# Kernel optimization log

Measured on AMD Instinct MI355X. Metric: run time of the kernel, lower is better.

Reference implementation:

```python
import jax, jax.numpy as jnp
import numpy as np

D_IN = 1024
D_OUT = 1024
NUM_HEADS = 16
HEAD_DIM = D_OUT // NUM_HEADS


def setup_inputs() -> dict:
    key = jax.random.key(0)
    ks = jax.random.split(key, 6)
    s = 0.02
    return {
        "x": jax.random.normal(ks[0], (4, 2048, D_IN), dtype=jnp.float32),
        "W_q": jax.random.normal(ks[1], (D_IN, D_OUT), dtype=jnp.float32) * s,
        "W_k": jax.random.normal(ks[2], (D_IN, D_OUT), dtype=jnp.float32) * s,
        "W_v": jax.random.normal(ks[3], (D_IN, D_OUT), dtype=jnp.float32) * s,
        "W_o": jax.random.normal(ks[4], (D_OUT, D_OUT), dtype=jnp.float32) * s,
        "b_o": jax.random.normal(ks[5], (D_OUT,), dtype=jnp.float32) * s,
    }


def reference(x, W_q, W_k, W_v, W_o, b_o):
    b, n, _ = x.shape
    # project and split heads: [b, h, n, d]
    q = (x @ W_q).reshape(b, n, NUM_HEADS, HEAD_DIM).transpose(0, 2, 1, 3)
    k = (x @ W_k).reshape(b, n, NUM_HEADS, HEAD_DIM).transpose(0, 2, 1, 3)
    v = (x @ W_v).reshape(b, n, NUM_HEADS, HEAD_DIM).transpose(0, 2, 1, 3)
    scores = jnp.einsum("bhqd,bhkd->bhqk", q, k)
    causal = jnp.tril(jnp.ones((n, n), dtype=bool))  # True = keep
    scores = jnp.where(causal, scores, -jnp.inf)
    attn = jax.nn.softmax(scores / np.sqrt(HEAD_DIM).astype(np.float32), axis=-1)
    ctx = jnp.einsum("bhqk,bhkd->bhqd", attn, v)
    ctx = ctx.transpose(0, 2, 1, 3).reshape(b, n, D_OUT)
    return ctx @ W_o + b_o
```

## Files before the change

kernel.cpp:

```cpp
#include <hip/hip_runtime.h>
#include <hip/hip_bf16.h>

#define NHEADS 16
#define HDIM 64
#define SEQ 2048
#define BATCH 4
#define DMODEL 1024
#define MTOT (BATCH * SEQ)

typedef short v8s __attribute__((ext_vector_type(8)));
typedef short v4s __attribute__((ext_vector_type(4)));
typedef float v4f __attribute__((ext_vector_type(4)));
typedef float v16f __attribute__((ext_vector_type(16)));
typedef unsigned int v4u __attribute__((ext_vector_type(4)));
typedef unsigned short u16;
typedef unsigned int u32;

__device__ __forceinline__ u16 f2bf(float f) {
    union { float f; unsigned u; } v; v.f = f;
    unsigned r = v.u + 0x7FFFu + ((v.u >> 16) & 1u);
    return (u16)(r >> 16);
}

__device__ __forceinline__ void g2l16(const u16* g, short* l) {
    __builtin_amdgcn_global_load_lds(
        (const __attribute__((address_space(1))) u32*)g,
        (__attribute__((address_space(3))) u32*)l, 16, 0, 0);
}

__device__ __forceinline__ unsigned pk_bf16(float a, float b) {
    unsigned r;
    asm("v_cvt_pk_bf16_f32 %0, %1, %2" : "=v"(r) : "v"(a), "v"(b));
    return r;
}
__device__ __forceinline__ void pl32swap(unsigned& x, unsigned& y) {
    asm("v_permlane32_swap_b32 %0, %1" : "+v"(x), "+v"(y));
}
__device__ __forceinline__ v8s build_pa(float a0, float a1, float a2, float a3,
                                        float b0, float b1, float b2, float b3) {
    unsigned X  = pk_bf16(a0, a1);
    unsigned X2 = pk_bf16(a2, a3);
    unsigned Y  = pk_bf16(b0, b1);
    unsigned Y2 = pk_bf16(b2, b3);
    pl32swap(X, Y);
    pl32swap(X2, Y2);
    v4u w; w[0] = X; w[1] = X2; w[2] = Y; w[3] = Y2;
    return __builtin_bit_cast(v8s, w);
}

__device__ __forceinline__ void transpose_body(
    const float* __restrict__ src, u16* __restrict__ dst, int k0, int n0)
{
    __shared__ __align__(8) short Ts[64 * 68];
    const int t = threadIdx.x;
    const int n4 = (t & 15) * 4, kl = t >> 4;
#pragma unroll
    for (int it = 0; it < 4; ++it) {
        int k = kl + 16 * it;
        v4f v = *(const v4f*)&src[(size_t)(k0 + k) * DMODEL + n0 + n4];
        v4s p;
#pragma unroll
        for (int e = 0; e < 4; ++e) p[e] = (short)f2bf(v[e]);
        *(v4s*)&Ts[k * 68 + n4] = p;
    }
    __syncthreads();
    const int nl = t >> 4, k4 = (t & 15) * 4;
#pragma unroll
    for (int it = 0; it < 4; ++it) {
        int n = nl + 16 * it;
        v4s o;
#pragma unroll
        for (int e = 0; e < 4; ++e) o[e] = Ts[(k4 + e) * 68 + n];
        *(v4s*)&dst[(size_t)(n0 + n) * DMODEL + k0 + k4] = o;
    }
}

__global__ __launch_bounds__(256)
void transpose_w(const float* __restrict__ src, u16* __restrict__ dst)
{
    transpose_body(src, dst, blockIdx.x * 64, blockIdx.y * 64);
}

__global__ __launch_bounds__(256)
void prep(const float* __restrict__ x, u16* __restrict__ xb,
          const float* __restrict__ s0, const float* __restrict__ s1,
          const float* __restrict__ s2, const float* __restrict__ s3,
          u16* __restrict__ wdst)
{
    const int blk = blockIdx.x;
    if (blk < 1024) {
        const int z = blk >> 8;
        const int rem = blk & 255;
        const float* src = (z == 0) ? s0 : (z == 1) ? s1 : (z == 2) ? s2 : s3;
        transpose_body(src, wdst + (size_t)z * DMODEL * DMODEL,
                       (rem & 15) * 64, (rem >> 4) * 64);
    } else {
        size_t i = ((size_t)(blk - 1024) * 256 + threadIdx.x) * 8;
        v4f a = *(const v4f*)&x[i];
        v4f b = *(const v4f*)&x[i + 4];
        v8s p;
#pragma unroll
        for (int e = 0; e < 4; ++e) p[e] = (short)f2bf(a[e]);
#pragma unroll
        for (int e = 0; e < 4; ++e) p[4 + e] = (short)f2bf(b[e]);
        *(v8s*)&xb[i] = p;
    }
}

#define QSCALE (0.125f * 1.44269504088896f)

__device__ __forceinline__ void qkv_epilogue(
    v4f (&acc)[4][4], int which, int n0, int m0, int wn, int wm,
    int l15, int quad, u16* Qb, u16* Kb, u16* Vt)
{
    if (which == 2) {
#pragma unroll
        for (int i = 0; i < 4; ++i)
#pragma unroll
            for (int j = 0; j < 4; ++j) {
                int col = n0 + wn + j * 16 + l15;
                int h = col >> 6, d = col & 63;
                int m = m0 + wm + i * 16 + quad * 4;
                int b = m >> 11, n = m & (SEQ - 1);
                v4s pv;
#pragma unroll
                for (int r = 0; r < 4; ++r) pv[r] = (short)f2bf(acc[i][j][r]);
                *(v4s*)&Vt[((size_t)(b * NHEADS + h) * HDIM + d) * SEQ + n] = pv;
            }
    } else {
        u16* Ob = (which == 0) ? Qb : Kb;
        const float scale = (which == 0) ? QSCALE : 1.0f;
#pragma unroll
        for (int i = 0; i < 4; ++i)
#pragma unroll
            for (int j = 0; j < 4; ++j) {
                int col = n0 + wn + j * 16 + l15;
                int h = col >> 6, d = col & 63;
#pragma unroll
                for (int r = 0; r < 4; ++r) {
                    int m = m0 + wm + i * 16 + quad * 4 + r;
                    int b = m >> 11, n = m & (SEQ - 1);
                    Ob[((size_t)(b * NHEADS + h) * SEQ + n) * HDIM + d] =
                        f2bf(acc[i][j][r] * scale);
                }
            }
    }
}

#define QKV_ABUF (256 * 64)
#define QKV_BBUF (128 * 64)

__device__ __forceinline__ void qkv_stage(
    const u16* __restrict__ xb, const u16* __restrict__ W,
    int m0, int t, int s, short* As3, short* Bs3)
{
    const int srr = t >> 3;
    const int scol = ((t & 7) ^ (srr & 7)) * 8;
    short* A = As3 + (s % 3) * QKV_ABUF;
    short* B = Bs3 + (s % 3) * QKV_BBUF;
    const int k0 = s * 64;
#pragma unroll
    for (int c = 0; c < 4; ++c)
        g2l16(&xb[(size_t)(m0 + c * 64 + srr) * DMODEL + k0 + scol],
              &A[(c * 64 + srr) * 64 + (t & 7) * 8]);
#pragma unroll
    for (int c = 0; c < 2; ++c)
        g2l16(&W[(size_t)(c * 64 + srr) * DMODEL + k0 + scol],
              &B[(c * 64 + srr) * 64 + (t & 7) * 8]);
}

__global__ __launch_bounds__(512, 1)
void qkv_fast(const u16* __restrict__ xb, const u16* __restrict__ Wt,
              u16* __restrict__ Qb, u16* __restrict__ Kb, u16* __restrict__ Vt)
{
    __shared__ __align__(16) short As3[3 * QKV_ABUF];
    __shared__ __align__(16) short Bs3[3 * QKV_BBUF];

    const int bx = blockIdx.x;
    const int which = bx >> 3;
    const int n0 = (bx & 7) * 128;
    const int m0 = blockIdx.y * 256;
    const u16* W = Wt + (size_t)which * DMODEL * DMODEL + (size_t)n0 * DMODEL;

    const int t = threadIdx.x;
    const int lane = t & 63;
    const int l15 = lane & 15;
    const int quad = lane >> 4;
    const int wave = t >> 6;
    const int wm = (wave >> 1) * 64;
    const int wn = (wave & 1) * 64;

    v4f acc[4][4];
#pragma unroll
    for (int i = 0; i < 4; ++i)
#pragma unroll
        for (int j = 0; j < 4; ++j) acc[i][j] = {0.f, 0.f, 0.f, 0.f};

    qkv_stage(xb, W, m0, t, 0, As3, Bs3);
    qkv_stage(xb, W, m0, t, 1, As3, Bs3);

#pragma unroll 1
    for (int tt = 0; tt < 16; ++tt) {
        if (tt < 15) asm volatile("s_waitcnt vmcnt(6)" ::: "memory");
        else         asm volatile("s_waitcnt vmcnt(0)" ::: "memory");
        __builtin_amdgcn_sched_barrier(0);
        __builtin_amdgcn_s_barrier();
        __builtin_amdgcn_sched_barrier(0);

        if (tt + 2 < 16) qkv_stage(xb, W, m0, t, tt + 2, As3, Bs3);

        const short* A = As3 + (tt % 3) * QKV_ABUF;
        const short* B = Bs3 + (tt % 3) * QKV_BBUF;
        v8s af[4][2], bf[4][2];
#pragma unroll
        for (int i = 0; i < 4; ++i)
#pragma unroll
            for (int kh = 0; kh < 2; ++kh)
                af[i][kh] = *(const v8s*)&A[(wm + i * 16 + l15) * 64 +
                                            (((kh * 4 + quad) ^ (l15 & 7)) << 3)];
#pragma unroll
        for (int j = 0; j < 4; ++j)
#pragma unroll
            for (int kh = 0; kh < 2; ++kh)
                bf[j][kh] = *(const v8s*)&B[(wn + j * 16 + l15) * 64 +
                                            (((kh * 4 + quad) ^ (l15 & 7)) << 3)];
        __builtin_amdgcn_s_setprio(1);
#pragma unroll
        for (int i = 0; i < 4; ++i)
#pragma unroll
            for (int j = 0; j < 4; ++j)
#pragma unroll
                for (int kh = 0; kh < 2; ++kh)
                    acc[i][j] = __builtin_amdgcn_mfma_f32_16x16x32_bf16(
                        af[i][kh], bf[j][kh], acc[i][j], 0, 0, 0);
        __builtin_amdgcn_s_setprio(0);
    }

    qkv_epilogue(acc, which, n0, m0, wn, wm, l15, quad, Qb, Kb, Vt);
}

__global__ __launch_bounds__(256, 2)
void qkv_slow(const float* __restrict__ x, const u16* __restrict__ Wt,
              u16* __restrict__ Qb, u16* __restrict__ Kb, u16* __restrict__ Vt)
{
    __shared__ __align__(16) short As[128 * 32];
    __shared__ __align__(16) short Bs[128 * 32];

    const int which = blockIdx.z;
    const u16* W = Wt + (size_t)which * DMODEL * DMODEL;

    const int n0 = blockIdx.x * 128;
    const int m0 = blockIdx.y * 128;
    const int t = threadIdx.x;
    const int lane = t & 63;
    const int l15 = lane & 15;
    const int quad = lane >> 4;
    const int wave = t >> 6;
    const int wm = (wave >> 1) * 64;
    const int wn = (wave & 1) * 64;
    const int srow = t >> 2;
    const int sc8 = (t & 3) * 8;

    v4f acc[4][4];
#pragma unroll
    for (int i = 0; i < 4; ++i)
#pragma unroll
        for (int j = 0; j < 4; ++j) acc[i][j] = {0.f, 0.f, 0.f, 0.f};

    for (int k0 = 0; k0 < DMODEL; k0 += 32) {
        __syncthreads();
        g2l16(&W[(size_t)(n0 + srow) * DMODEL + k0 + sc8], &Bs[srow * 32 + sc8]);
        g2l16(&W[(size_t)(n0 + 64 + srow) * DMODEL + k0 + sc8],
              &Bs[(64 + srow) * 32 + sc8]);
#pragma unroll
        for (int it = 0; it < 2; ++it) {
            int row = srow + 64 * it;
            const float* xp = &x[(size_t)(m0 + row) * DMODEL + k0 + sc8];
            v4f x0 = *(const v4f*)xp;
            v4f x1 = *(const v4f*)(xp + 4);
            v8s av;
#pragma unroll
            for (int e = 0; e < 4; ++e) av[e] = (short)f2bf(x0[e]);
#pragma unroll
            for (int e = 0; e < 4; ++e) av[4 + e] = (short)f2bf(x1[e]);
            *(v8s*)&As[row * 32 + sc8] = av;
        }
        __syncthreads();

        v8s af[4], bf[4];
#pragma unroll
        for (int i = 0; i < 4; ++i)
            af[i] = *(const v8s*)&As[(wm + i * 16 + l15) * 32 + quad * 8];
#pragma unroll
        for (int j = 0; j < 4; ++j)
            bf[j] = *(const v8s*)&Bs[(wn + j * 16 + l15) * 32 + quad * 8];
#pragma unroll
        for (int i = 0; i < 4; ++i)
#pragma unroll
            for (int j = 0; j < 4; ++j)
                acc[i][j] = __builtin_amdgcn_mfma_f32_16x16x32_bf16(
                    af[i], bf[j], acc[i][j], 0, 0, 0);
    }
    qkv_epilogue(acc, which, n0, m0, wn, wm, l15, quad, Qb, Kb, Vt);
}

#define VXOR(d) ((((d) & 7) << 1) | (((d) >> 3) & 1))

__global__ __launch_bounds__(256, 2)
void attn(const u16* __restrict__ Qb, const u16* __restrict__ Kb,
          const u16* __restrict__ Vt, u16* __restrict__ Cx)
{
    __shared__ __align__(16) short Ks[128 * 64];
    __shared__ __align__(16) short Vs[64 * 128];

    const int ell = blockIdx.x;
    const int xcd = ell & 7;
    const int rest = ell >> 3;
    const int p = rest & 7;
    const int bh = ((rest >> 3) << 3) | xcd;

    const int t = threadIdx.x;
    const int lane = t & 63;
    const int l31 = lane & 31;
    const int hi = lane >> 5;
    const int wave = t >> 6;
    const int koff = hi * 8;

    const u16* Qh = Qb + (size_t)bh * SEQ * HDIM;
    const u16* Kh = Kb + (size_t)bh * SEQ * HDIM;
    const u16* Vh = Vt + (size_t)bh * HDIM * SEQ;

    const int krow = t >> 3;
    const int kslot = t & 7;
    const int vrow = t >> 4;
    const int vslot = t & 15;
    const int b = bh >> 4, h = bh & 15;

#pragma unroll 1
    for (int phase = 0; phase < 2; ++phase) {
        const int qt = phase ? p : (15 - p);
        const int q0w = qt * 128 + wave * 32;

        v8s qf[4];
#pragma unroll
        for (int dc = 0; dc < 4; ++dc)
            qf[dc] = *(const v8s*)
                &Qh[(size_t)(q0w + l31) * HDIM + dc * 16 + koff];

        v16f o0, o1;
#pragma unroll
        for (int r = 0; r < 16; ++r) { o0[r] = 0.f; o1[r] = 0.f; }
        float ls = 0.f;

        v8s pk[4], pv[4];
#pragma unroll
        for (int it = 0; it < 4; ++it)
            pk[it] = *(const v8s*)
                &Kh[(size_t)(it * 32 + krow) * HDIM + kslot * 8];
#pragma unroll
        for (int it = 0; it < 4; ++it)
            pv[it] = *(const v8s*)
                &Vh[(size_t)(it * 16 + vrow) * SEQ + vslot * 8];

#pragma unroll 1
        for (int kb = 0; kb <= qt; ++kb) {
            __syncthreads();
#pragma unroll
            for (int it = 0; it < 4; ++it) {
                int row = it * 32 + krow;
                *(v8s*)&Ks[row * 64 + ((kslot ^ (row & 7)) << 3)] = pk[it];
            }
#pragma unroll
            for (int it = 0; it < 4; ++it) {
                int d = it * 16 + vrow;
                *(v8s*)&Vs[d * 128 + ((vslot ^ VXOR(d)) << 3)] = pv[it];
            }
            __syncthreads();

            if (kb < qt) {
                const int kn = (kb + 1) * 128;
#pragma unroll
                for (int it = 0; it < 4; ++it)
                    pk[it] = *(const v8s*)
                        &Kh[(size_t)(kn + it * 32 + krow) * HDIM + kslot * 8];
#pragma unroll
                for (int it = 0; it < 4; ++it)
                    pv[it] = *(const v8s*)
                        &Vh[(size_t)(it * 16 + vrow) * SEQ + kn + vslot * 8];
            }

#pragma unroll
            for (int k2 = 0; k2 < 2; ++k2) {
                const int kbase = kb * 128 + k2 * 64;
                if (kbase > q0w + 31) continue;
                const bool diag = (kbase + 63 > q0w);
                const int qrow = q0w + l31;

                v16f st0, st1;
#pragma unroll
                for (int r = 0; r < 16; ++r) { st0[r] = 0.f; st1[r] = 0.f; }
#pragma unroll
                for (int dc = 0; dc < 4; ++dc) {
                    const int ds = dc * 2 + hi;
                    const int r0 = k2 * 64 + l31;
                    const int r1 = k2 * 64 + 32 + l31;
                    v8s kf0 = *(const v8s*)
                        &Ks[r0 * 64 + ((ds ^ (r0 & 7)) << 3)];
                    v8s kf1 = *(const v8s*)
                        &Ks[r1 * 64 + ((ds ^ (r1 & 7)) << 3)];
                    st0 = __builtin_amdgcn_mfma_f32_32x32x16_bf16(
                        kf0, qf[dc], st0, 0, 0, 0);
                    st1 = __builtin_amdgcn_mfma_f32_32x32x16_bf16(
                        kf1, qf[dc], st1, 0, 0, 0);
                }

                v16f pe0, pe1;
                if (!diag) {
#pragma unroll
                    for (int r = 0; r < 16; ++r) {
                        pe0[r] = exp2f(st0[r]);
                        pe1[r] = exp2f(st1[r]);
                    }
                } else {
#pragma unroll
                    for (int r = 0; r < 16; ++r) {
                        int kl = kbase + (r & 3) + 8 * (r >> 2) + 4 * hi;
                        pe0[r] = (kl > qrow) ? 0.f : exp2f(st0[r]);
                        pe1[r] = (kl + 32 > qrow) ? 0.f : exp2f(st1[r]);
                    }
                }
#pragma unroll
                for (int r = 0; r < 16; ++r) ls += pe0[r] + pe1[r];

                v8s pa0 = build_pa(pe0[0], pe0[1], pe0[2], pe0[3],
                                   pe0[4], pe0[5], pe0[6], pe0[7]);
                v8s pa1 = build_pa(pe0[8], pe0[9], pe0[10], pe0[11],
                                   pe0[12], pe0[13], pe0[14], pe0[15]);
                v8s pa2 = build_pa(pe1[0], pe1[1], pe1[2], pe1[3],
                                   pe1[4], pe1[5], pe1[6], pe1[7]);
                v8s pa3 = build_pa(pe1[8], pe1[9], pe1[10], pe1[11],
                                   pe1[12], pe1[13], pe1[14], pe1[15]);

#pragma unroll
                for (int kc = 0; kc < 4; ++kc) {
                    v8s pav = (kc == 0) ? pa0 : (kc == 1) ? pa1
                              : (kc == 2) ? pa2 : pa3;
                    const int ks = k2 * 8 + kc * 2 + hi;
                    const int d0 = l31, d1 = 32 + l31;
                    v8s vf0 = *(const v8s*)
                        &Vs[d0 * 128 + ((ks ^ VXOR(d0)) << 3)];
                    v8s vf1 = *(const v8s*)
                        &Vs[d1 * 128 + ((ks ^ VXOR(d1)) << 3)];
                    o0 = __builtin_amdgcn_mfma_f32_32x32x16_bf16(
                        pav, vf0, o0, 0, 0, 0);
                    o1 = __builtin_amdgcn_mfma_f32_32x32x16_bf16(
                        pav, vf1, o1, 0, 0, 0);
                }
            }
        }

        ls += __shfl_xor(ls, 32, 64);
        float inv = 1.f / ls;
#pragma unroll
        for (int r = 0; r < 16; ++r) {
            int m = (r & 3) + 8 * (r >> 2) + 4 * hi;
            float im = __shfl(inv, m, 64);
            size_t idx = ((size_t)(b * SEQ + q0w + m)) * DMODEL
                         + h * HDIM + l31;
            Cx[idx] = f2bf(o0[r] * im);
            Cx[idx + 32] = f2bf(o1[r] * im);
        }
    }
}

__global__ __launch_bounds__(256, 2)
void out_gemm(const u16* __restrict__ Cx, const u16* __restrict__ WoT,
              const float* __restrict__ bo, float* __restrict__ Y)
{
    __shared__ __align__(16) short As[128 * 64];
    __shared__ __align__(16) short Bs[128 * 64];

    const int n0 = blockIdx.x * 128;
    const int m0 = blockIdx.y * 128;
    const int t = threadIdx.x;
    const int lane = t & 63;
    const int l15 = lane & 15;
    const int quad = lane >> 4;
    const int wave = t >> 6;
    const int wm = (wave >> 1) * 64;
    const int wn = (wave & 1) * 64;
    const int srow = t >> 3;
    const int sc8 = (t & 7) * 8;

    v4f acc[4][4];
#pragma unroll
    for (int i = 0; i < 4; ++i)
#pragma unroll
        for (int j = 0; j < 4; ++j) acc[i][j] = {0.f, 0.f, 0.f, 0.f};

    for (int k0 = 0; k0 < DMODEL; k0 += 64) {
        __syncthreads();
#pragma unroll
        for (int c = 0; c < 4; ++c) {
            g2l16(&Cx[(size_t)(m0 + c * 32 + srow) * DMODEL + k0 + sc8],
                  &As[(c * 32 + srow) * 64 + sc8]);
            g2l16(&WoT[(size_t)(n0 + c * 32 + srow) * DMODEL + k0 + sc8],
                  &Bs[(c * 32 + srow) * 64 + sc8]);
        }
        __syncthreads();

#pragma unroll
        for (int kh = 0; kh < 2; ++kh) {
            v8s af[4], bf[4];
#pragma unroll
            for (int i = 0; i < 4; ++i)
                af[i] = *(const v8s*)
                    &As[(wm + i * 16 + l15) * 64 + kh * 32 + quad * 8];
#pragma unroll
            for (int j = 0; j < 4; ++j)
                bf[j] = *(const v8s*)
                    &Bs[(wn + j * 16 + l15) * 64 + kh * 32 + quad * 8];
#pragma unroll
            for (int i = 0; i < 4; ++i)
#pragma unroll
                for (int j = 0; j < 4; ++j)
                    acc[i][j] = __builtin_amdgcn_mfma_f32_16x16x32_bf16(
                        af[i], bf[j], acc[i][j], 0, 0, 0);
        }
    }

#pragma unroll
    for (int i = 0; i < 4; ++i)
#pragma unroll
        for (int j = 0; j < 4; ++j) {
            int col = n0 + wn + j * 16 + l15;
            float bias = bo[col];
#pragma unroll
            for (int r = 0; r < 4; ++r) {
                int m = m0 + wm + i * 16 + quad * 4 + r;
                Y[(size_t)m * DMODEL + col] = acc[i][j][r] + bias;
            }
        }
}

extern "C" void kernel_launch(void* const* d_in, const int* in_sizes, int n_in,
                              void* d_out, int out_size, void* d_ws,
                              size_t ws_size, hipStream_t stream)
{
    const float* x  = (const float*)d_in[0];
    const float* Wq = (const float*)d_in[1];
    const float* Wk = (const float*)d_in[2];
    const float* Wv = (const float*)d_in[3];
    const float* Wo = (const float*)d_in[4];
    const float* bo = (const float*)d_in[5];
    float* Y = (float*)d_out;

    const size_t per = (size_t)BATCH * NHEADS * SEQ * HDIM;
    const size_t wsz = (size_t)DMODEL * DMODEL;
    u16* base = (u16*)d_ws;

    if (ws_size >= (size_t)72 * 1024 * 1024) {
        u16* xb  = base;
        u16* Cx  = base;
        u16* Wt4 = base + per;
        u16* Qb  = base + per + 4 * wsz;
        u16* Kb  = Qb + per;
        u16* Vt  = Kb + per;

        prep<<<1024 + MTOT * DMODEL / (256 * 8), 256, 0, stream>>>(
            x, xb, Wq, Wk, Wv, Wo, Wt4);
        qkv_fast<<<dim3(24, MTOT / 256), 512, 0, stream>>>(
            xb, Wt4, Qb, Kb, Vt);
        attn<<<512, 256, 0, stream>>>(Qb, Kb, Vt, Cx);
        out_gemm<<<dim3(DMODEL / 128, MTOT / 128), 256, 0, stream>>>(
            Cx, Wt4 + 3 * wsz, bo, Y);
    } else {
        u16* Wt  = base;
        u16* Cx  = base;
        u16* Qb  = base + per;
        u16* WoT = base + per;
        u16* Kb  = base + 2 * per;
        u16* Vt  = base + 3 * per;

        transpose_w<<<dim3(16, 16), 256, 0, stream>>>(Wq, Wt);
        transpose_w<<<dim3(16, 16), 256, 0, stream>>>(Wk, Wt + wsz);
        transpose_w<<<dim3(16, 16), 256, 0, stream>>>(Wv, Wt + 2 * wsz);
        qkv_slow<<<dim3(DMODEL / 128, MTOT / 128, 3), 256, 0, stream>>>(
            x, Wt, Qb, Kb, Vt);
        attn<<<512, 256, 0, stream>>>(Qb, Kb, Vt, Cx);
        transpose_w<<<dim3(16, 16), 256, 0, stream>>>(Wo, WoT);
        out_gemm<<<dim3(DMODEL / 128, MTOT / 128), 256, 0, stream>>>(
            Cx, WoT, bo, Y);
    }
}
```

Measured before the change: 259.7 us.

## Rework QKV GEMM with 32x32 MFMA split-stage pipeline and double-buffer attention K/V

```diff
diff --git a/kernel.cpp b/kernel.cpp
--- a/kernel.cpp
+++ b/kernel.cpp
@@ -109,6 +109,193 @@
 
 #define QSCALE (0.125f * 1.44269504088896f)
 
+#define QKV_ABUF (256 * 64)
+#define QKV_BBUF (128 * 64)
+
+__device__ __forceinline__ void qkv_stage3(
+    const u16* __restrict__ xb, const u16* __restrict__ W,
+    int m0, int t, int s, int part, short* As3, short* Bs3)
+{
+    const int srr = t >> 3;
+    const int scol = ((t & 7) ^ (srr & 7)) * 8;
+    short* A = As3 + (s % 3) * QKV_ABUF;
+    short* B = Bs3 + (s % 3) * QKV_BBUF;
+    const int k0 = s * 64;
+    if (part == 0) {
+        g2l16(&xb[(size_t)(m0 + srr) * DMODEL + k0 + scol], &A[t * 8]);
+        g2l16(&xb[(size_t)(m0 + 64 + srr) * DMODEL + k0 + scol],
+              &A[4096 + t * 8]);
+        g2l16(&W[(size_t)srr * DMODEL + k0 + scol], &B[t * 8]);
+    } else {
+        g2l16(&xb[(size_t)(m0 + 128 + srr) * DMODEL + k0 + scol],
+              &A[8192 + t * 8]);
+        g2l16(&xb[(size_t)(m0 + 192 + srr) * DMODEL + k0 + scol],
+              &A[12288 + t * 8]);
+        g2l16(&W[(size_t)(64 + srr) * DMODEL + k0 + scol], &B[4096 + t * 8]);
+    }
+}
+
+template <bool SW>
+__device__ __forceinline__ void qkv_loop32(
+    const u16* __restrict__ xb, const u16* __restrict__ W,
+    int m0, int t, short* As3, short* Bs3, v16f (&acc)[2][2])
+{
+    const int lane = t & 63;
+    const int l31 = lane & 31;
+    const int hi = lane >> 5;
+    const int wave = t >> 6;
+    const int wm = (wave >> 1) * 64;
+    const int wn = (wave & 1) * 64;
+    const int x7 = l31 & 7;
+
+    qkv_stage3(xb, W, m0, t, 0, 0, As3, Bs3);
+    qkv_stage3(xb, W, m0, t, 0, 1, As3, Bs3);
+    qkv_stage3(xb, W, m0, t, 1, 0, As3, Bs3);
+    qkv_stage3(xb, W, m0, t, 1, 1, As3, Bs3);
+    asm volatile("s_waitcnt vmcnt(6)" ::: "memory");
+    __builtin_amdgcn_sched_barrier(0);
+    __builtin_amdgcn_s_barrier();
+    __builtin_amdgcn_sched_barrier(0);
+
+#pragma unroll 1
+    for (int tt = 0; tt < 16; ++tt) {
+        const short* A = As3 + (tt % 3) * QKV_ABUF;
+        const short* B = Bs3 + (tt % 3) * QKV_BBUF;
+        v8s af[2][2], bf[2][2];
+
+#pragma unroll
+        for (int i = 0; i < 2; ++i)
+#pragma unroll
+            for (int ks = 0; ks < 2; ++ks) {
+                af[i][ks] = *(const v8s*)&A[(wm + i * 32 + l31) * 64 +
+                                            (((ks * 2 + hi) ^ x7) << 3)];
+                bf[i][ks] = *(const v8s*)&B[(wn + i * 32 + l31) * 64 +
+                                            (((ks * 2 + hi) ^ x7) << 3)];
+            }
+        if (tt + 2 < 16) qkv_stage3(xb, W, m0, t, tt + 2, 0, As3, Bs3);
+        __builtin_amdgcn_s_barrier();
+        asm volatile("s_waitcnt lgkmcnt(0)" ::: "memory");
+        __builtin_amdgcn_sched_barrier(0);
+        __builtin_amdgcn_s_setprio(1);
+#pragma unroll
+        for (int i = 0; i < 2; ++i)
+#pragma unroll
+            for (int j = 0; j < 2; ++j)
+#pragma unroll
+                for (int ks = 0; ks < 2; ++ks) {
+                    if (SW)
+                        acc[i][j] = __builtin_amdgcn_mfma_f32_32x32x16_bf16(
+                            bf[j][ks], af[i][ks], acc[i][j], 0, 0, 0);
+                    else
+                        acc[i][j] = __builtin_amdgcn_mfma_f32_32x32x16_bf16(
+                            af[i][ks], bf[j][ks], acc[i][j], 0, 0, 0);
+                }
+        __builtin_amdgcn_s_setprio(0);
+        __builtin_amdgcn_s_barrier();
+
+#pragma unroll
+        for (int i = 0; i < 2; ++i)
+#pragma unroll
+            for (int ks = 0; ks < 2; ++ks) {
+                af[i][ks] = *(const v8s*)&A[(wm + i * 32 + l31) * 64 +
+                                            ((((ks + 2) * 2 + hi) ^ x7) << 3)];
+                bf[i][ks] = *(const v8s*)&B[(wn + i * 32 + l31) * 64 +
+                                            ((((ks + 2) * 2 + hi) ^ x7) << 3)];
+            }
+        if (tt + 2 < 16) qkv_stage3(xb, W, m0, t, tt + 2, 1, As3, Bs3);
+        __builtin_amdgcn_s_barrier();
+        asm volatile("s_waitcnt lgkmcnt(0)" ::: "memory");
+        __builtin_amdgcn_sched_barrier(0);
+        __builtin_amdgcn_s_setprio(1);
+#pragma unroll
+        for (int i = 0; i < 2; ++i)
+#pragma unroll
+            for (int j = 0; j < 2; ++j)
+#pragma unroll
+                for (int ks = 0; ks < 2; ++ks) {
+                    if (SW)
+                        acc[i][j] = __builtin_amdgcn_mfma_f32_32x32x16_bf16(
+                            bf[j][ks], af[i][ks], acc[i][j], 0, 0, 0);
+                    else
+                        acc[i][j] = __builtin_amdgcn_mfma_f32_32x32x16_bf16(
+                            af[i][ks], bf[j][ks], acc[i][j], 0, 0, 0);
+                }
+        __builtin_amdgcn_s_setprio(0);
+        if (tt < 14)       asm volatile("s_waitcnt vmcnt(6)" ::: "memory");
+        else if (tt == 14) asm volatile("s_waitcnt vmcnt(0)" ::: "memory");
+        __builtin_amdgcn_sched_barrier(0);
+        __builtin_amdgcn_s_barrier();
+        __builtin_amdgcn_sched_barrier(0);
+    }
+}
+
+__global__ __launch_bounds__(512, 1)
+void qkv_fast(const u16* __restrict__ xb, const u16* __restrict__ Wt,
+              u16* __restrict__ Qb, u16* __restrict__ Kb, u16* __restrict__ Vt)
+{
+    __shared__ __align__(16) short As3[3 * QKV_ABUF];
+    __shared__ __align__(16) short Bs3[3 * QKV_BBUF];
+
+    const int bx = blockIdx.x;
+    const int which = bx >> 3;
+    const int n0 = (bx & 7) * 128;
+    const int m0 = blockIdx.y * 256;
+    const u16* W = Wt + (size_t)which * DMODEL * DMODEL + (size_t)n0 * DMODEL;
+
+    const int t = threadIdx.x;
+    const int lane = t & 63;
+    const int l31 = lane & 31;
+    const int hi = lane >> 5;
+    const int wave = t >> 6;
+    const int wm = (wave >> 1) * 64;
+    const int wn = (wave & 1) * 64;
+
+    v16f acc[2][2];
+#pragma unroll
+    for (int i = 0; i < 2; ++i)
+#pragma unroll
+        for (int j = 0; j < 2; ++j)
+#pragma unroll
+            for (int r = 0; r < 16; ++r) acc[i][j][r] = 0.f;
+
+    if (which == 2) {
+        qkv_loop32<true>(xb, W, m0, t, As3, Bs3, acc);
+#pragma unroll
+        for (int i = 0; i < 2; ++i) {
+            int m = m0 + wm + i * 32 + l31;
+            int b = m >> 11, n = m & (SEQ - 1);
+#pragma unroll
+            for (int j = 0; j < 2; ++j)
+#pragma unroll
+                for (int r = 0; r < 16; ++r) {
+                    int ncol = n0 + wn + j * 32 + (r & 3) + 8 * (r >> 2)
+                               + 4 * hi;
+                    int h = ncol >> 6, d = ncol & 63;
+                    Vt[((size_t)(b * NHEADS + h) * HDIM + d) * SEQ + n] =
+                        f2bf(acc[i][j][r]);
+                }
+        }
+    } else {
+        qkv_loop32<false>(xb, W, m0, t, As3, Bs3, acc);
+        u16* Ob = which ? Kb : Qb;
+        const float scale = which ? 1.0f : QSCALE;
+#pragma unroll
+        for (int j = 0; j < 2; ++j) {
+            int col = n0 + wn + j * 32 + l31;
+            int h = col >> 6, d = col & 63;
+#pragma unroll
+            for (int i = 0; i < 2; ++i)
+#pragma unroll
+                for (int r = 0; r < 16; ++r) {
+                    int m = m0 + wm + i * 32 + (r & 3) + 8 * (r >> 2) + 4 * hi;
+                    int b = m >> 11, n = m & (SEQ - 1);
+                    Ob[((size_t)(b * NHEADS + h) * SEQ + n) * HDIM + d] =
+                        f2bf(acc[i][j][r] * scale);
+                }
+        }
+    }
+}
+
 __device__ __forceinline__ void qkv_epilogue(
     v4f (&acc)[4][4], int which, int n0, int m0, int wn, int wm,
     int l15, int quad, u16* Qb, u16* Kb, u16* Vt)
@@ -145,98 +332,6 @@
                 }
             }
     }
-}
-
-#define QKV_ABUF (256 * 64)
-#define QKV_BBUF (128 * 64)
-
-__device__ __forceinline__ void qkv_stage(
-    const u16* __restrict__ xb, const u16* __restrict__ W,
-    int m0, int t, int s, short* As3, short* Bs3)
-{
-    const int srr = t >> 3;
-    const int scol = ((t & 7) ^ (srr & 7)) * 8;
-    short* A = As3 + (s % 3) * QKV_ABUF;
-    short* B = Bs3 + (s % 3) * QKV_BBUF;
-    const int k0 = s * 64;
-#pragma unroll
-    for (int c = 0; c < 4; ++c)
-        g2l16(&xb[(size_t)(m0 + c * 64 + srr) * DMODEL + k0 + scol],
-              &A[(c * 64 + srr) * 64 + (t & 7) * 8]);
-#pragma unroll
-    for (int c = 0; c < 2; ++c)
-        g2l16(&W[(size_t)(c * 64 + srr) * DMODEL + k0 + scol],
-              &B[(c * 64 + srr) * 64 + (t & 7) * 8]);
-}
-
-__global__ __launch_bounds__(512, 1)
-void qkv_fast(const u16* __restrict__ xb, const u16* __restrict__ Wt,
-              u16* __restrict__ Qb, u16* __restrict__ Kb, u16* __restrict__ Vt)
-{
-    __shared__ __align__(16) short As3[3 * QKV_ABUF];
-    __shared__ __align__(16) short Bs3[3 * QKV_BBUF];
-
-    const int bx = blockIdx.x;
-    const int which = bx >> 3;
-    const int n0 = (bx & 7) * 128;
-    const int m0 = blockIdx.y * 256;
-    const u16* W = Wt + (size_t)which * DMODEL * DMODEL + (size_t)n0 * DMODEL;
-
-    const int t = threadIdx.x;
-    const int lane = t & 63;
-    const int l15 = lane & 15;
-    const int quad = lane >> 4;
-    const int wave = t >> 6;
-    const int wm = (wave >> 1) * 64;
-    const int wn = (wave & 1) * 64;
-
-    v4f acc[4][4];
-#pragma unroll
-    for (int i = 0; i < 4; ++i)
-#pragma unroll
-        for (int j = 0; j < 4; ++j) acc[i][j] = {0.f, 0.f, 0.f, 0.f};
-
-    qkv_stage(xb, W, m0, t, 0, As3, Bs3);
-    qkv_stage(xb, W, m0, t, 1, As3, Bs3);
-
-#pragma unroll 1
-    for (int tt = 0; tt < 16; ++tt) {
-        if (tt < 15) asm volatile("s_waitcnt vmcnt(6)" ::: "memory");
-        else         asm volatile("s_waitcnt vmcnt(0)" ::: "memory");
-        __builtin_amdgcn_sched_barrier(0);
-        __builtin_amdgcn_s_barrier();
-        __builtin_amdgcn_sched_barrier(0);
-
-        if (tt + 2 < 16) qkv_stage(xb, W, m0, t, tt + 2, As3, Bs3);
-
-        const short* A = As3 + (tt % 3) * QKV_ABUF;
-        const short* B = Bs3 + (tt % 3) * QKV_BBUF;
-        v8s af[4][2], bf[4][2];
-#pragma unroll
-        for (int i = 0; i < 4; ++i)
-#pragma unroll
-            for (int kh = 0; kh < 2; ++kh)
-                af[i][kh] = *(const v8s*)&A[(wm + i * 16 + l15) * 64 +
-                                            (((kh * 4 + quad) ^ (l15 & 7)) << 3)];
-#pragma unroll
-        for (int j = 0; j < 4; ++j)
-#pragma unroll
-            for (int kh = 0; kh < 2; ++kh)
-                bf[j][kh] = *(const v8s*)&B[(wn + j * 16 + l15) * 64 +
-                                            (((kh * 4 + quad) ^ (l15 & 7)) << 3)];
-        __builtin_amdgcn_s_setprio(1);
-#pragma unroll
-        for (int i = 0; i < 4; ++i)
-#pragma unroll
-            for (int j = 0; j < 4; ++j)
-#pragma unroll
-                for (int kh = 0; kh < 2; ++kh)
-                    acc[i][j] = __builtin_amdgcn_mfma_f32_16x16x32_bf16(
-                        af[i][kh], bf[j][kh], acc[i][j], 0, 0, 0);
-        __builtin_amdgcn_s_setprio(0);
-    }
-
-    qkv_epilogue(acc, which, n0, m0, wn, wm, l15, quad, Qb, Kb, Vt);
 }
 
 __global__ __launch_bounds__(256, 2)
@@ -310,8 +405,8 @@
 void attn(const u16* __restrict__ Qb, const u16* __restrict__ Kb,
           const u16* __restrict__ Vt, u16* __restrict__ Cx)
 {
-    __shared__ __align__(16) short Ks[128 * 64];
-    __shared__ __align__(16) short Vs[64 * 128];
+    __shared__ __align__(16) short Ks[2][128 * 64];
+    __shared__ __align__(16) short Vs[2][64 * 128];
 
     const int ell = blockIdx.x;
     const int xcd = ell & 7;
@@ -361,21 +456,21 @@
         for (int it = 0; it < 4; ++it)
             pv[it] = *(const v8s*)
                 &Vh[(size_t)(it * 16 + vrow) * SEQ + vslot * 8];
+#pragma unroll
+        for (int it = 0; it < 4; ++it) {
+            int row = it * 32 + krow;
+            *(v8s*)&Ks[0][row * 64 + ((kslot ^ (row & 7)) << 3)] = pk[it];
+        }
+#pragma unroll
+        for (int it = 0; it < 4; ++it) {
+            int d = it * 16 + vrow;
+            *(v8s*)&Vs[0][d * 128 + ((vslot ^ VXOR(d)) << 3)] = pv[it];
+        }
+        __syncthreads();
 
 #pragma unroll 1
         for (int kb = 0; kb <= qt; ++kb) {
-            __syncthreads();
-#pragma unroll
-            for (int it = 0; it < 4; ++it) {
-                int row = it * 32 + krow;
-                *(v8s*)&Ks[row * 64 + ((kslot ^ (row & 7)) << 3)] = pk[it];
-            }
-#pragma unroll
-            for (int it = 0; it < 4; ++it) {
-                int d = it * 16 + vrow;
-                *(v8s*)&Vs[d * 128 + ((vslot ^ VXOR(d)) << 3)] = pv[it];
-            }
-            __syncthreads();
+            const int cur = kb & 1;
 
             if (kb < qt) {
                 const int kn = (kb + 1) * 128;
@@ -405,9 +500,9 @@
                     const int r0 = k2 * 64 + l31;
                     const int r1 = k2 * 64 + 32 + l31;
                     v8s kf0 = *(const v8s*)
-                        &Ks[r0 * 64 + ((ds ^ (r0 & 7)) << 3)];
+                        &Ks[cur][r0 * 64 + ((ds ^ (r0 & 7)) << 3)];
                     v8s kf1 = *(const v8s*)
-                        &Ks[r1 * 64 + ((ds ^ (r1 & 7)) << 3)];
+                        &Ks[cur][r1 * 64 + ((ds ^ (r1 & 7)) << 3)];
                     st0 = __builtin_amdgcn_mfma_f32_32x32x16_bf16(
                         kf0, qf[dc], st0, 0, 0, 0);
                     st1 = __builtin_amdgcn_mfma_f32_32x32x16_bf16(
@@ -448,15 +543,31 @@
                     const int ks = k2 * 8 + kc * 2 + hi;
                     const int d0 = l31, d1 = 32 + l31;
                     v8s vf0 = *(const v8s*)
-                        &Vs[d0 * 128 + ((ks ^ VXOR(d0)) << 3)];
+                        &Vs[cur][d0 * 128 + ((ks ^ VXOR(d0)) << 3)];
                     v8s vf1 = *(const v8s*)
-                        &Vs[d1 * 128 + ((ks ^ VXOR(d1)) << 3)];
+                        &Vs[cur][d1 * 128 + ((ks ^ VXOR(d1)) << 3)];
                     o0 = __builtin_amdgcn_mfma_f32_32x32x16_bf16(
                         pav, vf0, o0, 0, 0, 0);
                     o1 = __builtin_amdgcn_mfma_f32_32x32x16_bf16(
                         pav, vf1, o1, 0, 0, 0);
                 }
             }
+
+            if (kb < qt) {
+#pragma unroll
+                for (int it = 0; it < 4; ++it) {
+                    int row = it * 32 + krow;
+                    *(v8s*)&Ks[cur ^ 1][row * 64 + ((kslot ^ (row & 7)) << 3)]
+                        = pk[it];
+                }
+#pragma unroll
+                for (int it = 0; it < 4; ++it) {
+                    int d = it * 16 + vrow;
+                    *(v8s*)&Vs[cur ^ 1][d * 128 + ((vslot ^ VXOR(d)) << 3)]
+                        = pv[it];
+                }
+            }
+            __syncthreads();
         }
 
         ls += __shfl_xor(ls, 32, 64);
```

New measurement: 265.8 us. +2.3%, slower.
